# Performance work log

Hardware: AMD Instinct MI355X
Metric: run time of the kernel (lower is better)

Reference implementation:

```python
import jax, jax.numpy as jnp
import numpy as np

RX, RY, RZ = 32, 32, 32
NORMALIZE = True
EPS = 0.0


def setup_inputs() -> dict:
    key = jax.random.key(0)
    k1, k2 = jax.random.split(key)
    features = jax.random.normal(k1, (16, 64, 65536), dtype=jnp.float32)  # [B, C, N]
    coords = jax.random.normal(k2, (16, 3, 65536), dtype=jnp.float32)     # [B, 3, N]
    return {"features": features, "coords": coords}


def _norm_and_voxel_coords(coords):
    # coords: [B, 3, N]
    nc = coords - coords.mean(axis=2, keepdims=True)
    if NORMALIZE:
        # per-point L2 norm over xyz (dim 1), max over points (dim 2)
        norm = jnp.linalg.norm(nc, axis=1, keepdims=True)            # [B, 1, N]
        denom = norm.max(axis=2, keepdims=True) * 2.0 + EPS          # [B, 1, 1]
        nc = nc / denom + 0.5
    else:
        nc = (nc + 1.0) / 2.0
    r = jnp.array([RX, RY, RZ], dtype=nc.dtype).reshape(1, 3, 1)
    nc = jnp.clip(nc * r, 0.0, r - 1.0)                              # per-axis clamp
    vox = jnp.round(nc).astype(jnp.int32)                            # [B, 3, N]
    return vox, nc


def _avg_voxelize(features, vox):
    # features: [B, C, N], vox: [B, 3, N] int32 -> [B, C, RX, RY, RZ]
    B, C, N = features.shape
    R = RX * RY * RZ
    idx = vox[:, 0] * (RY * RZ) + vox[:, 1] * RZ + vox[:, 2]          # [B, N]
    flat_idx = (idx + jnp.arange(B, dtype=jnp.int32)[:, None] * R).reshape(-1)  # [B*N]
    feats = features.transpose(0, 2, 1).reshape(B * N, C)             # [B*N, C]
    sums = jax.ops.segment_sum(feats, flat_idx, num_segments=B * R)   # [B*R, C]
    cnts = jax.ops.segment_sum(jnp.ones((B * N,), features.dtype), flat_idx,
                               num_segments=B * R)                    # [B*R]
    avg = sums / jnp.maximum(cnts, 1.0)[:, None]
    return avg.reshape(B, RX, RY, RZ, C).transpose(0, 4, 1, 2, 3)


def reference(features, coords):
    vox, norm_coords = _norm_and_voxel_coords(coords)
    out = _avg_voxelize(features, vox)
    return out, norm_coords
```

## Files before the change

kernel.cpp:

```cpp
#include <hip/hip_runtime.h>

#define BATCH 16
#define CH 64
#define NPTS 65536
#define RX 32
#define RY 32
#define RZ 32
#define RVOX (RX * RY * RZ)
#define HALFVOX (RVOX / 2)
#define NQ (NPTS / 4)

__global__ void mean_kernel(const float* __restrict__ coords, double* __restrict__ meanAcc) {
    const int b = blockIdx.y;
    const int t = blockIdx.x * blockDim.x + threadIdx.x;
    const float4* cb = (const float4*)(coords + (size_t)b * 3 * NPTS);
    double s[3];
#pragma unroll
    for (int d = 0; d < 3; ++d) {
        const float4 v = cb[d * NQ + t];
        s[d] = ((double)v.x + (double)v.y) + ((double)v.z + (double)v.w);
    }
#pragma unroll
    for (int off = 32; off > 0; off >>= 1) {
        s[0] += __shfl_down(s[0], off);
        s[1] += __shfl_down(s[1], off);
        s[2] += __shfl_down(s[2], off);
    }
    __shared__ double red[3][4];
    const int wave = threadIdx.x >> 6, lane = threadIdx.x & 63;
    if (lane == 0) { red[0][wave] = s[0]; red[1][wave] = s[1]; red[2][wave] = s[2]; }
    __syncthreads();
    if (threadIdx.x == 0) {
        double tx = 0, ty = 0, tz = 0;
        for (int w = 0; w < 4; ++w) { tx += red[0][w]; ty += red[1][w]; tz += red[2][w]; }
        atomicAdd(&meanAcc[b * 3 + 0], tx);
        atomicAdd(&meanAcc[b * 3 + 1], ty);
        atomicAdd(&meanAcc[b * 3 + 2], tz);
    }
}

__global__ void maxnorm_kernel(const float* __restrict__ coords,
                               const double* __restrict__ meanAcc,
                               int* __restrict__ maxAcc) {
    const int b = blockIdx.y;
    const int t = blockIdx.x * blockDim.x + threadIdx.x;
    const float4* cb = (const float4*)(coords + (size_t)b * 3 * NPTS);
    const float mx = (float)(meanAcc[b * 3 + 0] * (1.0 / NPTS));
    const float my = (float)(meanAcc[b * 3 + 1] * (1.0 / NPTS));
    const float mz = (float)(meanAcc[b * 3 + 2] * (1.0 / NPTS));
    const float4 x = cb[0 * NQ + t];
    const float4 y = cb[1 * NQ + t];
    const float4 z = cb[2 * NQ + t];
    float m = 0.0f;
    {
        float dx = x.x - mx, dy = y.x - my, dz = z.x - mz; m = fmaxf(m, dx*dx + dy*dy + dz*dz);
        dx = x.y - mx; dy = y.y - my; dz = z.y - mz;      m = fmaxf(m, dx*dx + dy*dy + dz*dz);
        dx = x.z - mx; dy = y.z - my; dz = z.z - mz;      m = fmaxf(m, dx*dx + dy*dy + dz*dz);
        dx = x.w - mx; dy = y.w - my; dz = z.w - mz;      m = fmaxf(m, dx*dx + dy*dy + dz*dz);
    }
#pragma unroll
    for (int off = 32; off > 0; off >>= 1) m = fmaxf(m, __shfl_down(m, off));
    __shared__ float redm[4];
    const int wave = threadIdx.x >> 6, lane = threadIdx.x & 63;
    if (lane == 0) redm[wave] = m;
    __syncthreads();
    if (threadIdx.x == 0) {
        float tmax = fmaxf(fmaxf(redm[0], redm[1]), fmaxf(redm[2], redm[3]));
        atomicMax(&maxAcc[b], __float_as_int(tmax));
    }
}

__global__ void point_kernel(const float* __restrict__ coords,
                             const double* __restrict__ meanAcc,
                             const int* __restrict__ maxAcc,
                             float* __restrict__ normc,
                             unsigned short* __restrict__ idx16,
                             float* __restrict__ counts) {
    const int t = blockIdx.x * blockDim.x + threadIdx.x;
    const int b = t >> 14;
    const int q = t & (NQ - 1);
    const float denom = 2.0f * sqrtf(__int_as_float(maxAcc[b]));
    const float4* cb = (const float4*)(coords + (size_t)b * 3 * NPTS);
    float4* nb = (float4*)(normc + (size_t)b * 3 * NPTS);
    int vx[3][4];
#pragma unroll
    for (int d = 0; d < 3; ++d) {
        const float m = (float)(meanAcc[b * 3 + d] * (1.0 / NPTS));
        float4 v = cb[d * NQ + q];
        float4 s;
        s.x = fminf(fmaxf(((v.x - m) / denom + 0.5f) * 32.0f, 0.0f), 31.0f);
        s.y = fminf(fmaxf(((v.y - m) / denom + 0.5f) * 32.0f, 0.0f), 31.0f);
        s.z = fminf(fmaxf(((v.z - m) / denom + 0.5f) * 32.0f, 0.0f), 31.0f);
        s.w = fminf(fmaxf(((v.w - m) / denom + 0.5f) * 32.0f, 0.0f), 31.0f);
        nb[d * NQ + q] = s;
        vx[d][0] = (int)rintf(s.x);
        vx[d][1] = (int)rintf(s.y);
        vx[d][2] = (int)rintf(s.z);
        vx[d][3] = (int)rintf(s.w);
    }
    ushort4 o;
    o.x = (unsigned short)(vx[0][0] * (RY * RZ) + vx[1][0] * RZ + vx[2][0]);
    o.y = (unsigned short)(vx[0][1] * (RY * RZ) + vx[1][1] * RZ + vx[2][1]);
    o.z = (unsigned short)(vx[0][2] * (RY * RZ) + vx[1][2] * RZ + vx[2][2]);
    o.w = (unsigned short)(vx[0][3] * (RY * RZ) + vx[1][3] * RZ + vx[2][3]);
    ((ushort4*)(idx16 + (size_t)b * NPTS))[q] = o;
    float* cbp = counts + (size_t)b * RVOX;
    atomicAdd(&cbp[o.x], 1.0f);
    atomicAdd(&cbp[o.y], 1.0f);
    atomicAdd(&cbp[o.z], 1.0f);
    atomicAdd(&cbp[o.w], 1.0f);
}

__global__ __launch_bounds__(1024) void accum_kernel(const float* __restrict__ features,
                                                     const unsigned short* __restrict__ idx16,
                                                     const float* __restrict__ counts,
                                                     float* __restrict__ out) {
    __shared__ float g[HALFVOX];
    const int c = blockIdx.x;
    const int b = blockIdx.y;
    const int tid = threadIdx.x;
    const float4* fs = (const float4*)(features + ((size_t)(b * CH + c)) * NPTS);
    const ushort4* is = (const ushort4*)(idx16 + (size_t)b * NPTS);
    const float* cb = counts + (size_t)b * RVOX;
    float* ob = out + ((size_t)(b * CH + c)) * RVOX;

#pragma unroll
    for (int half = 0; half < 2; ++half) {
        for (int i = tid; i < HALFVOX; i += 1024) g[i] = 0.0f;
        __syncthreads();
        const unsigned short want = (unsigned short)half;
        for (int base = tid; base < NQ; base += 4096) {
            const float4 f0 = fs[base];
            const float4 f1 = fs[base + 1024];
            const float4 f2 = fs[base + 2048];
            const float4 f3 = fs[base + 3072];
            const ushort4 v0 = is[base];
            const ushort4 v1 = is[base + 1024];
            const ushort4 v2 = is[base + 2048];
            const ushort4 v3 = is[base + 3072];
            if ((v0.x >> 14) == want) atomicAdd(&g[v0.x & (HALFVOX - 1)], f0.x);
            if ((v0.y >> 14) == want) atomicAdd(&g[v0.y & (HALFVOX - 1)], f0.y);
            if ((v0.z >> 14) == want) atomicAdd(&g[v0.z & (HALFVOX - 1)], f0.z);
            if ((v0.w >> 14) == want) atomicAdd(&g[v0.w & (HALFVOX - 1)], f0.w);
            if ((v1.x >> 14) == want) atomicAdd(&g[v1.x & (HALFVOX - 1)], f1.x);
            if ((v1.y >> 14) == want) atomicAdd(&g[v1.y & (HALFVOX - 1)], f1.y);
            if ((v1.z >> 14) == want) atomicAdd(&g[v1.z & (HALFVOX - 1)], f1.z);
            if ((v1.w >> 14) == want) atomicAdd(&g[v1.w & (HALFVOX - 1)], f1.w);
            if ((v2.x >> 14) == want) atomicAdd(&g[v2.x & (HALFVOX - 1)], f2.x);
            if ((v2.y >> 14) == want) atomicAdd(&g[v2.y & (HALFVOX - 1)], f2.y);
            if ((v2.z >> 14) == want) atomicAdd(&g[v2.z & (HALFVOX - 1)], f2.z);
            if ((v2.w >> 14) == want) atomicAdd(&g[v2.w & (HALFVOX - 1)], f2.w);
            if ((v3.x >> 14) == want) atomicAdd(&g[v3.x & (HALFVOX - 1)], f3.x);
            if ((v3.y >> 14) == want) atomicAdd(&g[v3.y & (HALFVOX - 1)], f3.y);
            if ((v3.z >> 14) == want) atomicAdd(&g[v3.z & (HALFVOX - 1)], f3.z);
            if ((v3.w >> 14) == want) atomicAdd(&g[v3.w & (HALFVOX - 1)], f3.w);
        }
        __syncthreads();
        const float* ch = cb + half * HALFVOX;
        float* oh = ob + half * HALFVOX;
        for (int i = tid; i < HALFVOX / 4; i += 1024) {
            const float4 c4 = ((const float4*)ch)[i];
            float4 v = ((const float4*)g)[i];
            v.x /= fmaxf(c4.x, 1.0f);
            v.y /= fmaxf(c4.y, 1.0f);
            v.z /= fmaxf(c4.z, 1.0f);
            v.w /= fmaxf(c4.w, 1.0f);
            ((float4*)oh)[i] = v;
        }
        __syncthreads();
    }
}

extern "C" void kernel_launch(void* const* d_in, const int* in_sizes, int n_in,
                              void* d_out, int out_size, void* d_ws, size_t ws_size,
                              hipStream_t stream) {
    const float* features = (const float*)d_in[0];
    const float* coords = (const float*)d_in[1];
    float* out = (float*)d_out;
    float* normc = out + (size_t)BATCH * CH * RVOX;

    char* ws = (char*)d_ws;
    double* meanAcc = (double*)ws;
    int* maxAcc = (int*)(ws + 384);
    float* counts = (float*)(ws + 512);
    unsigned short* idx16 = (unsigned short*)(ws + 512 + (size_t)BATCH * RVOX * 4);

    hipMemsetAsync(ws, 0, 512 + (size_t)BATCH * RVOX * 4, stream);

    dim3 gred(NQ / 256, BATCH);
    mean_kernel<<<gred, 256, 0, stream>>>(coords, meanAcc);
    maxnorm_kernel<<<gred, 256, 0, stream>>>(coords, meanAcc, maxAcc);

    point_kernel<<<(BATCH * NQ) / 256, 256, 0, stream>>>(coords, meanAcc, maxAcc,
                                                         normc, idx16, counts);

    accum_kernel<<<dim3(CH, BATCH), 1024, 0, stream>>>(features, idx16, counts, out);
}
```

Measured before the change: 729.3 us.

## Move voxel counting to shared-memory kernel and software-pipeline accum loads

Removes the global float atomics for voxel counts from point_kernel and adds a count_kernel that builds per-batch histograms in LDS using packed 16-bit counters. This lets the large counts memset go away. The accum kernel moves to 512 threads with launch bounds for 4 blocks per CU, and double-buffers its feature and index loads in registers so global loads overlap the LDS atomics. The risks are higher register pressure and a count_kernel with only 16 blocks, which leaves most CUs idle while it runs.

Result: no change. 730.6 us (+0.2%).

```diff
diff --git a/kernel.cpp b/kernel.cpp
--- a/kernel.cpp
+++ b/kernel.cpp
@@ -74,8 +74,7 @@
                              const double* __restrict__ meanAcc,
                              const int* __restrict__ maxAcc,
                              float* __restrict__ normc,
-                             unsigned short* __restrict__ idx16,
-                             float* __restrict__ counts) {
+                             unsigned short* __restrict__ idx16) {
     const int t = blockIdx.x * blockDim.x + threadIdx.x;
     const int b = t >> 14;
     const int q = t & (NQ - 1);
@@ -104,17 +103,35 @@
     o.z = (unsigned short)(vx[0][2] * (RY * RZ) + vx[1][2] * RZ + vx[2][2]);
     o.w = (unsigned short)(vx[0][3] * (RY * RZ) + vx[1][3] * RZ + vx[2][3]);
     ((ushort4*)(idx16 + (size_t)b * NPTS))[q] = o;
-    float* cbp = counts + (size_t)b * RVOX;
-    atomicAdd(&cbp[o.x], 1.0f);
-    atomicAdd(&cbp[o.y], 1.0f);
-    atomicAdd(&cbp[o.z], 1.0f);
-    atomicAdd(&cbp[o.w], 1.0f);
-}
-
-__global__ __launch_bounds__(1024) void accum_kernel(const float* __restrict__ features,
-                                                     const unsigned short* __restrict__ idx16,
-                                                     const float* __restrict__ counts,
-                                                     float* __restrict__ out) {
+}
+
+__global__ __launch_bounds__(1024) void count_kernel(const unsigned short* __restrict__ idx16,
+                                                     float* __restrict__ counts) {
+    __shared__ unsigned int cnt[RVOX / 2];
+    const int b = blockIdx.x;
+    const int tid = threadIdx.x;
+    for (int i = tid; i < RVOX / 2; i += 1024) cnt[i] = 0u;
+    __syncthreads();
+    const ushort4* is = (const ushort4*)(idx16 + (size_t)b * NPTS);
+#pragma unroll 4
+    for (int i = tid; i < NQ; i += 1024) {
+        const ushort4 v = is[i];
+        atomicAdd(&cnt[v.x >> 1], 1u << ((v.x & 1) * 16));
+        atomicAdd(&cnt[v.y >> 1], 1u << ((v.y & 1) * 16));
+        atomicAdd(&cnt[v.z >> 1], 1u << ((v.z & 1) * 16));
+        atomicAdd(&cnt[v.w >> 1], 1u << ((v.w & 1) * 16));
+    }
+    __syncthreads();
+    float* cb = counts + (size_t)b * RVOX;
+    for (int i = tid; i < RVOX; i += 1024) {
+        cb[i] = (float)((cnt[i >> 1] >> ((i & 1) * 16)) & 0xFFFFu);
+    }
+}
+
+__global__ __launch_bounds__(512, 4) void accum_kernel(const float* __restrict__ features,
+                                                       const unsigned short* __restrict__ idx16,
+                                                       const float* __restrict__ counts,
+                                                       float* __restrict__ out) {
     __shared__ float g[HALFVOX];
     const int c = blockIdx.x;
     const int b = blockIdx.y;
@@ -126,39 +143,41 @@
 
 #pragma unroll
     for (int half = 0; half < 2; ++half) {
-        for (int i = tid; i < HALFVOX; i += 1024) g[i] = 0.0f;
+        for (int i = tid; i < HALFVOX / 4; i += 512) ((float4*)g)[i] = make_float4(0, 0, 0, 0);
         __syncthreads();
         const unsigned short want = (unsigned short)half;
-        for (int base = tid; base < NQ; base += 4096) {
-            const float4 f0 = fs[base];
-            const float4 f1 = fs[base + 1024];
-            const float4 f2 = fs[base + 2048];
-            const float4 f3 = fs[base + 3072];
-            const ushort4 v0 = is[base];
-            const ushort4 v1 = is[base + 1024];
-            const ushort4 v2 = is[base + 2048];
-            const ushort4 v3 = is[base + 3072];
-            if ((v0.x >> 14) == want) atomicAdd(&g[v0.x & (HALFVOX - 1)], f0.x);
-            if ((v0.y >> 14) == want) atomicAdd(&g[v0.y & (HALFVOX - 1)], f0.y);
-            if ((v0.z >> 14) == want) atomicAdd(&g[v0.z & (HALFVOX - 1)], f0.z);
-            if ((v0.w >> 14) == want) atomicAdd(&g[v0.w & (HALFVOX - 1)], f0.w);
-            if ((v1.x >> 14) == want) atomicAdd(&g[v1.x & (HALFVOX - 1)], f1.x);
-            if ((v1.y >> 14) == want) atomicAdd(&g[v1.y & (HALFVOX - 1)], f1.y);
-            if ((v1.z >> 14) == want) atomicAdd(&g[v1.z & (HALFVOX - 1)], f1.z);
-            if ((v1.w >> 14) == want) atomicAdd(&g[v1.w & (HALFVOX - 1)], f1.w);
-            if ((v2.x >> 14) == want) atomicAdd(&g[v2.x & (HALFVOX - 1)], f2.x);
-            if ((v2.y >> 14) == want) atomicAdd(&g[v2.y & (HALFVOX - 1)], f2.y);
-            if ((v2.z >> 14) == want) atomicAdd(&g[v2.z & (HALFVOX - 1)], f2.z);
-            if ((v2.w >> 14) == want) atomicAdd(&g[v2.w & (HALFVOX - 1)], f2.w);
-            if ((v3.x >> 14) == want) atomicAdd(&g[v3.x & (HALFVOX - 1)], f3.x);
-            if ((v3.y >> 14) == want) atomicAdd(&g[v3.y & (HALFVOX - 1)], f3.y);
-            if ((v3.z >> 14) == want) atomicAdd(&g[v3.z & (HALFVOX - 1)], f3.z);
-            if ((v3.w >> 14) == want) atomicAdd(&g[v3.w & (HALFVOX - 1)], f3.w);
+
+        float4 F[2][8];
+        ushort4 I[2][8];
+#pragma unroll
+        for (int j = 0; j < 8; ++j) {
+            F[0][j] = fs[tid + j * 512];
+            I[0][j] = is[tid + j * 512];
+        }
+#pragma unroll
+        for (int grp = 0; grp < 4; ++grp) {
+            const int cur = grp & 1, nxt = cur ^ 1;
+            if (grp < 3) {
+#pragma unroll
+                for (int j = 0; j < 8; ++j) {
+                    F[nxt][j] = fs[tid + ((grp + 1) * 8 + j) * 512];
+                    I[nxt][j] = is[tid + ((grp + 1) * 8 + j) * 512];
+                }
+            }
+#pragma unroll
+            for (int j = 0; j < 8; ++j) {
+                const float4 f = F[cur][j];
+                const ushort4 v = I[cur][j];
+                if ((v.x >> 14) == want) atomicAdd(&g[v.x & (HALFVOX - 1)], f.x);
+                if ((v.y >> 14) == want) atomicAdd(&g[v.y & (HALFVOX - 1)], f.y);
+                if ((v.z >> 14) == want) atomicAdd(&g[v.z & (HALFVOX - 1)], f.z);
+                if ((v.w >> 14) == want) atomicAdd(&g[v.w & (HALFVOX - 1)], f.w);
+            }
         }
         __syncthreads();
         const float* ch = cb + half * HALFVOX;
         float* oh = ob + half * HALFVOX;
-        for (int i = tid; i < HALFVOX / 4; i += 1024) {
+        for (int i = tid; i < HALFVOX / 4; i += 512) {
             const float4 c4 = ((const float4*)ch)[i];
             float4 v = ((const float4*)g)[i];
             v.x /= fmaxf(c4.x, 1.0f);
@@ -185,14 +204,16 @@
     float* counts = (float*)(ws + 512);
     unsigned short* idx16 = (unsigned short*)(ws + 512 + (size_t)BATCH * RVOX * 4);
 
-    hipMemsetAsync(ws, 0, 512 + (size_t)BATCH * RVOX * 4, stream);
+    hipMemsetAsync(ws, 0, 512, stream);
 
     dim3 gred(NQ / 256, BATCH);
     mean_kernel<<<gred, 256, 0, stream>>>(coords, meanAcc);
     maxnorm_kernel<<<gred, 256, 0, stream>>>(coords, meanAcc, maxAcc);
 
     point_kernel<<<(BATCH * NQ) / 256, 256, 0, stream>>>(coords, meanAcc, maxAcc,
-                                                         normc, idx16, counts);
-
-    accum_kernel<<<dim3(CH, BATCH), 1024, 0, stream>>>(features, idx16, counts, out);
-}
+                                                         normc, idx16);
+
+    count_kernel<<<BATCH, 1024, 0, stream>>>(idx16, counts);
+
+    accum_kernel<<<dim3(CH, BATCH), 512, 0, stream>>>(features, idx16, counts, out);
+}
```
